# Kernel optimization log

Hardware: AMD Instinct MI355X
Metric: run time of the kernel (lower is better)

## Reference

```python
import jax, jax.numpy as jnp
import numpy as np

BATCH, LENGTH, IN, STATE, OUT = 8, 4096, 512, 256, 512


def setup_inputs() -> dict:
    key = jax.random.key(0)
    k1, k2, k3, k4, k5 = jax.random.split(key, 5)
    u = jax.random.normal(k1, (BATCH, LENGTH, IN), dtype=jnp.float32)
    x0 = jax.random.normal(k2, (BATCH, STATE), dtype=jnp.float32)
    A = 0.9999 * (2.0 * jax.random.uniform(k3, (STATE,), dtype=jnp.float32) - 1.0)
    B = jax.random.normal(k4, (IN, STATE), dtype=jnp.float32) / (STATE + IN) ** 0.5
    C = jax.random.normal(k5, (STATE, OUT), dtype=jnp.float32) / STATE ** 0.5
    return {"u": u, "x0": x0, "A": A, "B": B, "C": C}


def reference(u, x0, A, B, C):
    L = u.shape[1]
    # A_powers[t, n] = A[n] ** t, shape [L, state]
    A_powers = jnp.power(A[None, :], jnp.arange(L, dtype=u.dtype)[:, None])
    uB = u @ B  # [batch, L, state]
    # FFT convolution; inputs are real so rfft/irfft gives same result as
    # real(ifft(fft*fft)) in the original.
    T = 2 ** int(np.ceil(np.log2(2 * L - 1)))
    Af = jnp.fft.rfft(A_powers, n=T, axis=0)  # [T/2+1, state]
    Uf = jnp.fft.rfft(uB, n=T, axis=1)        # [batch, T/2+1, state]
    x = jnp.fft.irfft(Af[None, :, :] * Uf, n=T, axis=1)[:, :L]  # [batch, L, state]
    # initial-state contribution: A * A_powers * x0
    x = x + A[None, None, :] * A_powers[None, :, :] * x0[:, None, :]
    y = x @ C  # [batch, L, out]
    return (y, x[:, -1])
```

## Files before the change

### kernel.cpp

```cpp
#include <hip/hip_runtime.h>

#define BATCH   8
#define LENGTH  4096
#define IN_DIM  512
#define STATE   256
#define OUT_DIM 512
#define NC      256
#define LC      16

typedef __attribute__((ext_vector_type(8))) short bf16x8;
typedef __attribute__((ext_vector_type(4))) float f32x4;
typedef __attribute__((ext_vector_type(4))) unsigned short u16x4;

union FragU { bf16x8 v; unsigned u[4]; };

__device__ __forceinline__ unsigned short bf16_rne(float v) {
    unsigned u = __builtin_bit_cast(unsigned, v);
    unsigned r = (u + 0x7FFFu + ((u >> 16) & 1u)) >> 16;
    return (unsigned short)r;
}
__device__ __forceinline__ float bf16_f(unsigned short h) {
    unsigned u = ((unsigned)h) << 16;
    return __builtin_bit_cast(float, u);
}

__global__ __launch_bounds__(256) void split_weights(
    const float* __restrict__ B, const float* __restrict__ C,
    unsigned short* __restrict__ Bhi, unsigned short* __restrict__ Blo,
    unsigned short* __restrict__ Chi, unsigned short* __restrict__ Clo)
{
    int id = blockIdx.x * 256 + threadIdx.x;
    if (id < IN_DIM * STATE) {
        int k = id & (IN_DIM - 1), n = id >> 9;
        float v = B[(size_t)k * STATE + n];
        unsigned short h = bf16_rne(v);
        Bhi[id] = h;
        Blo[id] = bf16_rne(v - bf16_f(h));
    } else {
        int id2 = id - IN_DIM * STATE;
        int k = id2 & (STATE - 1), n = id2 >> 8;
        float v = C[(size_t)k * OUT_DIM + n];
        unsigned short h = bf16_rne(v);
        Chi[id2] = h;
        Clo[id2] = bf16_rne(v - bf16_f(h));
    }
}

__global__ __launch_bounds__(512, 4) void gemm_dbuf(
    const float* __restrict__ Af, const unsigned short* __restrict__ Bthi,
    const unsigned short* __restrict__ Btlo, float* __restrict__ Cc,
    int N_, int K)
{
    __shared__ unsigned short lds[2 * 16384];

    const int tid  = threadIdx.x;
    const int wave = tid >> 6;
    const int lane = tid & 63;
    const int n0 = blockIdx.x * 128;
    const int m0 = blockIdx.y * 128;

    const char* gp[4];
    int ldsoff[4], gstep[4];
    #pragma unroll
    for (int t = 0; t < 4; ++t) {
        int gi = wave * 4 + t;
        if (gi < 16) {
            int p = gi * 64 + lane;
            int row = p >> 3, s = p & 7;
            int l = s ^ (row & 7);
            gp[t] = (const char*)(Af + (size_t)(m0 + row) * K + l * 4);
            gstep[t] = 32 * 4;
            ldsoff[t] = gi * 512;
        } else {
            int q2 = (gi - 16) >> 3;
            int pi = gi & 7;
            int p = pi * 64 + lane;
            int row = p >> 2, s = p & 3;
            int l = s ^ ((row >> 1) & 3);
            const unsigned short* base = q2 ? Btlo : Bthi;
            gp[t] = (const char*)(base + (size_t)(n0 + row) * K + l * 8);
            gstep[t] = 32 * 2;
            ldsoff[t] = 8192 + q2 * 4096 + pi * 512;
        }
    }

    const int r = lane & 15, q = lane >> 4;
    const int wm = (wave >> 1) * 32, wn = (wave & 1) * 64;

    int aoff[2][2], boff[4];
    #pragma unroll
    for (int i = 0; i < 2; ++i) {
        int row = wm + i * 16 + r;
        #pragma unroll
        for (int h = 0; h < 2; ++h)
            aoff[i][h] = row * 64 + ((2 * q + h) ^ (row & 7)) * 8;
    }
    #pragma unroll
    for (int j = 0; j < 4; ++j) {
        int row = wn + j * 16 + r;
        boff[j] = row * 32 + (q ^ ((row >> 1) & 3)) * 8;
    }

    f32x4 acc[2][4];
    #pragma unroll
    for (int i = 0; i < 2; ++i)
        #pragma unroll
        for (int j = 0; j < 4; ++j)
            acc[i][j] = (f32x4){0.f, 0.f, 0.f, 0.f};

    #pragma unroll
    for (int t = 0; t < 4; ++t) {
        __builtin_amdgcn_global_load_lds(
            (const __attribute__((address_space(1))) unsigned*)(gp[t]),
            (__attribute__((address_space(3))) unsigned*)(&lds[ldsoff[t]]),
            16, 0, 0);
        gp[t] += gstep[t];
    }

    const int nit = K >> 5;
    for (int it = 0; it < nit; ++it) {
        asm volatile("" ::: "memory");
        __builtin_amdgcn_s_barrier();
        asm volatile("" ::: "memory");
        if (it + 1 < nit) {
            const int bb = ((it + 1) & 1) * 16384;
            #pragma unroll
            for (int t = 0; t < 4; ++t) {
                __builtin_amdgcn_global_load_lds(
                    (const __attribute__((address_space(1))) unsigned*)(gp[t]),
                    (__attribute__((address_space(3))) unsigned*)(&lds[bb + ldsoff[t]]),
                    16, 0, 0);
                gp[t] += gstep[t];
            }
            __builtin_amdgcn_s_waitcnt(0x0F74);
        } else {
            __builtin_amdgcn_s_waitcnt(0x0F70);
        }
        asm volatile("" ::: "memory");
        __builtin_amdgcn_s_barrier();
        asm volatile("" ::: "memory");

        const unsigned short* buf = &lds[(it & 1) * 16384];

        FragU ahi[2], alo[2];
        #pragma unroll
        for (int i = 0; i < 2; ++i) {
            #pragma unroll
            for (int h = 0; h < 2; ++h) {
                float4 f = *(const float4*)(buf + aoff[i][h]);
                unsigned bx = __builtin_bit_cast(unsigned, f.x);
                unsigned by = __builtin_bit_cast(unsigned, f.y);
                unsigned bz = __builtin_bit_cast(unsigned, f.z);
                unsigned bw = __builtin_bit_cast(unsigned, f.w);
                ahi[i].u[h * 2]     = __builtin_amdgcn_perm(by, bx, 0x07060302);
                ahi[i].u[h * 2 + 1] = __builtin_amdgcn_perm(bw, bz, 0x07060302);
                float lx = f.x - __builtin_bit_cast(float, bx & 0xFFFF0000u);
                float ly = f.y - __builtin_bit_cast(float, by & 0xFFFF0000u);
                float lz = f.z - __builtin_bit_cast(float, bz & 0xFFFF0000u);
                float lw = f.w - __builtin_bit_cast(float, bw & 0xFFFF0000u);
                alo[i].u[h * 2]     = __builtin_amdgcn_perm(
                    __builtin_bit_cast(unsigned, ly), __builtin_bit_cast(unsigned, lx), 0x07060302);
                alo[i].u[h * 2 + 1] = __builtin_amdgcn_perm(
                    __builtin_bit_cast(unsigned, lw), __builtin_bit_cast(unsigned, lz), 0x07060302);
            }
        }
        FragU bhi[4], blo[4];
        #pragma unroll
        for (int j = 0; j < 4; ++j) {
            bhi[j].v = *(const bf16x8*)(buf +  8192 + boff[j]);
            blo[j].v = *(const bf16x8*)(buf + 12288 + boff[j]);
        }
        #pragma unroll
        for (int i = 0; i < 2; ++i)
            #pragma unroll
            for (int j = 0; j < 4; ++j) {
                acc[i][j] = __builtin_amdgcn_mfma_f32_16x16x32_bf16(ahi[i].v, bhi[j].v, acc[i][j], 0, 0, 0);
                acc[i][j] = __builtin_amdgcn_mfma_f32_16x16x32_bf16(alo[i].v, bhi[j].v, acc[i][j], 0, 0, 0);
                acc[i][j] = __builtin_amdgcn_mfma_f32_16x16x32_bf16(ahi[i].v, blo[j].v, acc[i][j], 0, 0, 0);
            }
    }

    #pragma unroll
    for (int i = 0; i < 2; ++i) {
        #pragma unroll
        for (int reg = 0; reg < 4; ++reg) {
            int mg = m0 + wm + i * 16 + q * 4 + reg;
            float* dst = Cc + (size_t)mg * N_ + n0 + wn + r;
            dst[0]  = acc[i][0][reg];
            dst[16] = acc[i][1][reg];
            dst[32] = acc[i][2][reg];
            dst[48] = acc[i][3][reg];
        }
    }
}

__global__ __launch_bounds__(512, 4) void gemm_presplit(
    const unsigned short* __restrict__ Athi, const unsigned short* __restrict__ Atlo,
    const unsigned short* __restrict__ Bthi, const unsigned short* __restrict__ Btlo,
    float* __restrict__ Cc, int N_, int K)
{
    __shared__ unsigned short lds[2 * 16384];

    const int tid  = threadIdx.x;
    const int wave = tid >> 6;
    const int lane = tid & 63;
    const int n0 = blockIdx.x * 128;
    const int m0 = blockIdx.y * 128;

    const char* gp[4];
    int ldsoff[4];
    #pragma unroll
    for (int t = 0; t < 4; ++t) {
        int gi = wave * 4 + t;
        int plane = gi >> 3;
        int pi = gi & 7;
        int p = pi * 64 + lane;
        int row = p >> 2, s = p & 3;
        int l = s ^ ((row >> 1) & 3);
        const unsigned short* base =
            (plane == 0) ? Athi : (plane == 1) ? Atlo : (plane == 2) ? Bthi : Btlo;
        int r0 = (plane < 2) ? m0 : n0;
        gp[t] = (const char*)(base + (size_t)(r0 + row) * K + l * 8);
        ldsoff[t] = plane * 4096 + pi * 512;
    }

    const int r = lane & 15, q = lane >> 4;
    const int wm = (wave >> 2) * 64, wn = (wave & 3) * 32;

    int aoff[4], boff[2];
    #pragma unroll
    for (int i = 0; i < 4; ++i) {
        int row = wm + i * 16 + r;
        aoff[i] = row * 32 + (q ^ ((row >> 1) & 3)) * 8;
    }
    #pragma unroll
    for (int j = 0; j < 2; ++j) {
        int row = wn + j * 16 + r;
        boff[j] = row * 32 + (q ^ ((row >> 1) & 3)) * 8;
    }

    f32x4 acc[4][2];
    #pragma unroll
    for (int i = 0; i < 4; ++i)
        #pragma unroll
        for (int j = 0; j < 2; ++j)
            acc[i][j] = (f32x4){0.f, 0.f, 0.f, 0.f};

    #pragma unroll
    for (int t = 0; t < 4; ++t) {
        __builtin_amdgcn_global_load_lds(
            (const __attribute__((address_space(1))) unsigned*)(gp[t]),
            (__attribute__((address_space(3))) unsigned*)(&lds[ldsoff[t]]),
            16, 0, 0);
        gp[t] += 64;
    }

    const int nit = K >> 5;
    for (int it = 0; it < nit; ++it) {
        asm volatile("" ::: "memory");
        __builtin_amdgcn_s_barrier();
        asm volatile("" ::: "memory");
        if (it + 1 < nit) {
            const int bb = ((it + 1) & 1) * 16384;
            #pragma unroll
            for (int t = 0; t < 4; ++t) {
                __builtin_amdgcn_global_load_lds(
                    (const __attribute__((address_space(1))) unsigned*)(gp[t]),
                    (__attribute__((address_space(3))) unsigned*)(&lds[bb + ldsoff[t]]),
                    16, 0, 0);
                gp[t] += 64;
            }
            __builtin_amdgcn_s_waitcnt(0x0F74);
        } else {
            __builtin_amdgcn_s_waitcnt(0x0F70);
        }
        asm volatile("" ::: "memory");
        __builtin_amdgcn_s_barrier();
        asm volatile("" ::: "memory");

        const unsigned short* buf = &lds[(it & 1) * 16384];

        FragU ahi[4], alo[4];
        #pragma unroll
        for (int i = 0; i < 4; ++i) {
            ahi[i].v = *(const bf16x8*)(buf +        aoff[i]);
            alo[i].v = *(const bf16x8*)(buf + 4096 + aoff[i]);
        }
        FragU bhi[2], blo[2];
        #pragma unroll
        for (int j = 0; j < 2; ++j) {
            bhi[j].v = *(const bf16x8*)(buf +  8192 + boff[j]);
            blo[j].v = *(const bf16x8*)(buf + 12288 + boff[j]);
        }
        #pragma unroll
        for (int i = 0; i < 4; ++i)
            #pragma unroll
            for (int j = 0; j < 2; ++j) {
                acc[i][j] = __builtin_amdgcn_mfma_f32_16x16x32_bf16(ahi[i].v, bhi[j].v, acc[i][j], 0, 0, 0);
                acc[i][j] = __builtin_amdgcn_mfma_f32_16x16x32_bf16(alo[i].v, bhi[j].v, acc[i][j], 0, 0, 0);
                acc[i][j] = __builtin_amdgcn_mfma_f32_16x16x32_bf16(ahi[i].v, blo[j].v, acc[i][j], 0, 0, 0);
            }
    }

    #pragma unroll
    for (int i = 0; i < 4; ++i) {
        #pragma unroll
        for (int reg = 0; reg < 4; ++reg) {
            int mg = m0 + wm + i * 16 + q * 4 + reg;
            float* dst = Cc + (size_t)mg * N_ + n0 + wn + r;
            dst[0]  = acc[i][0][reg];
            dst[16] = acc[i][1][reg];
        }
    }
}

__global__ __launch_bounds__(64) void scan_carry(
    const float* __restrict__ uB, const float* __restrict__ A,
    float* __restrict__ carry)
{
    const int b = blockIdx.x;
    const int c = blockIdx.y;
    const int t = threadIdx.x;
    const float4 a = *(const float4*)(A + 4 * t);
    const float4* p = (const float4*)(uB + ((size_t)b * LENGTH + (size_t)c * LC) * STATE) + t;
    float4 s = make_float4(0.f, 0.f, 0.f, 0.f);
    #pragma unroll
    for (int j = 0; j < LC; ++j) {
        float4 v = p[(size_t)j * (STATE / 4)];
        s.x = fmaf(a.x, s.x, v.x);
        s.y = fmaf(a.y, s.y, v.y);
        s.z = fmaf(a.z, s.z, v.z);
        s.w = fmaf(a.w, s.w, v.w);
    }
    *((float4*)(carry + ((size_t)b * NC + c) * STATE) + t) = s;
}

__global__ __launch_bounds__(256) void scan_entries(
    const float* __restrict__ carry, const float* __restrict__ A,
    const float* __restrict__ x0, float* __restrict__ entry)
{
    const int b = blockIdx.x;
    const int n = threadIdx.x;
    const float a = A[n];
    float aL = a;
    #pragma unroll
    for (int k = 0; k < 4; ++k) aL *= aL;

    float s = x0[(size_t)b * STATE + n];
    const float* cr = carry + (size_t)b * NC * STATE + n;
    float* en = entry + (size_t)b * NC * STATE + n;
    #pragma unroll 8
    for (int c = 0; c < NC; ++c) {
        en[(size_t)c * STATE] = s;
        s = fmaf(aL, s, cr[(size_t)c * STATE]);
    }
}

__global__ __launch_bounds__(64) void scan_apply(
    const float* __restrict__ uB, const float* __restrict__ A,
    const float* __restrict__ entry,
    unsigned short* __restrict__ xhi, unsigned short* __restrict__ xlo,
    float* __restrict__ x_last)
{
    const int b = blockIdx.x;
    const int c = blockIdx.y;
    const int t = threadIdx.x;
    const float4 a = *(const float4*)(A + 4 * t);

    float4 s = *((const float4*)(entry + ((size_t)b * NC + c) * STATE) + t);

    const size_t base = ((size_t)b * LENGTH + (size_t)c * LC) * STATE;
    const float4* p = (const float4*)(uB + base) + t;
    u16x4* qh = (u16x4*)(xhi + base) + t;
    u16x4* ql = (u16x4*)(xlo + base) + t;
    #pragma unroll
    for (int j = 0; j < LC; ++j) {
        float4 v = p[(size_t)j * (STATE / 4)];
        s.x = fmaf(a.x, s.x, v.x);
        s.y = fmaf(a.y, s.y, v.y);
        s.z = fmaf(a.z, s.z, v.z);
        s.w = fmaf(a.w, s.w, v.w);
        u16x4 hh, ll;
        unsigned ux = __builtin_bit_cast(unsigned, s.x);
        unsigned uy = __builtin_bit_cast(unsigned, s.y);
        unsigned uz = __builtin_bit_cast(unsigned, s.z);
        unsigned uw = __builtin_bit_cast(unsigned, s.w);
        hh[0] = (unsigned short)(ux >> 16);
        hh[1] = (unsigned short)(uy >> 16);
        hh[2] = (unsigned short)(uz >> 16);
        hh[3] = (unsigned short)(uw >> 16);
        float lx = s.x - __builtin_bit_cast(float, ux & 0xFFFF0000u);
        float ly = s.y - __builtin_bit_cast(float, uy & 0xFFFF0000u);
        float lz = s.z - __builtin_bit_cast(float, uz & 0xFFFF0000u);
        float lw = s.w - __builtin_bit_cast(float, uw & 0xFFFF0000u);
        ll[0] = (unsigned short)(__builtin_bit_cast(unsigned, lx) >> 16);
        ll[1] = (unsigned short)(__builtin_bit_cast(unsigned, ly) >> 16);
        ll[2] = (unsigned short)(__builtin_bit_cast(unsigned, lz) >> 16);
        ll[3] = (unsigned short)(__builtin_bit_cast(unsigned, lw) >> 16);
        qh[(size_t)j * (STATE / 4)] = hh;
        ql[(size_t)j * (STATE / 4)] = ll;
    }
    if (c == NC - 1)
        *((float4*)(x_last + (size_t)b * STATE) + t) = s;
}

extern "C" void kernel_launch(void* const* d_in, const int* in_sizes, int n_in,
                              void* d_out, int out_size, void* d_ws, size_t ws_size,
                              hipStream_t stream)
{
    const float* u  = (const float*)d_in[0];
    const float* x0 = (const float*)d_in[1];
    const float* A  = (const float*)d_in[2];
    const float* B  = (const float*)d_in[3];
    const float* C  = (const float*)d_in[4];

    const size_t MB = 1024 * 1024;
    char* ws = (char*)d_ws;

    unsigned short* xhi = (unsigned short*)(ws);
    unsigned short* xlo = (unsigned short*)(ws + 16 * MB);
    float* carry = (float*)(ws + 32 * MB);
    float* entry = (float*)(ws + 34 * MB);
    unsigned short* Bt_hi = (unsigned short*)(ws + 36 * MB);
    unsigned short* Bt_lo = (unsigned short*)(ws + 36 * MB + 256 * 1024);
    unsigned short* Ct_hi = (unsigned short*)(ws + 36 * MB + 512 * 1024);
    unsigned short* Ct_lo = (unsigned short*)(ws + 36 * MB + 768 * 1024);

    float* y      = (float*)d_out;
    float* x_last = y + (size_t)BATCH * LENGTH * OUT_DIM;
    float* uB     = (float*)((char*)d_out + 32 * MB);

    const int M = BATCH * LENGTH;

    split_weights<<<dim3((IN_DIM * STATE + STATE * OUT_DIM) / 256), dim3(256), 0, stream>>>(
        B, C, Bt_hi, Bt_lo, Ct_hi, Ct_lo);

    gemm_dbuf<<<dim3(STATE / 128, M / 128), dim3(512), 0, stream>>>(
        u, Bt_hi, Bt_lo, uB, STATE, IN_DIM);

    scan_carry<<<dim3(BATCH, NC), dim3(64), 0, stream>>>(uB, A, carry);
    scan_entries<<<dim3(BATCH), dim3(256), 0, stream>>>(carry, A, x0, entry);
    scan_apply<<<dim3(BATCH, NC), dim3(64), 0, stream>>>(uB, A, entry, xhi, xlo, x_last);

    gemm_presplit<<<dim3(OUT_DIM / 128, M / 128), dim3(512), 0, stream>>>(
        xhi, xlo, Ct_hi, Ct_lo, y, OUT_DIM, STATE);
}
```

Baseline: 208.7 us.

## Fuse chunk-carry scan reduction into uB GEMM epilogue; prefetch uB in scan_apply

Computes the per-chunk scan carries directly from the GEMM accumulators in the gemm_dbuf epilogue. Each 16-row chunk is weighted by powers of A and reduced across lanes with shuffles, which removes the separate scan_carry kernel and its full re-read of uB. scan_apply now loads all 16 uB rows into registers before the recurrence so the loads can be in flight together. The cost is extra epilogue work and register pressure in the GEMM, more registers in scan_apply, and summation-order differences in the carries.

```diff
diff --git a/kernel.cpp b/kernel.cpp
--- a/kernel.cpp
+++ b/kernel.cpp
@@ -49,6 +49,7 @@
 __global__ __launch_bounds__(512, 4) void gemm_dbuf(
     const float* __restrict__ Af, const unsigned short* __restrict__ Bthi,
     const unsigned short* __restrict__ Btlo, float* __restrict__ Cc,
+    const float* __restrict__ Av, float* __restrict__ carry,
     int N_, int K)
 {
     __shared__ unsigned short lds[2 * 16384];
@@ -192,6 +193,28 @@
             dst[48] = acc[i][3][reg];
         }
     }
+
+    {
+        const int b  = m0 >> 12;
+        const int c0 = ((m0 & 4095) + wm) >> 4;
+        #pragma unroll
+        for (int j = 0; j < 4; ++j) {
+            const int n = n0 + wn + j * 16 + r;
+            const float a  = Av[n];
+            const float a2 = a * a, a3 = a2 * a, a4 = a2 * a2;
+            const float a8 = a4 * a4, a12 = a8 * a4;
+            const float base = (q == 0) ? a12 : (q == 1) ? a8 : (q == 2) ? a4 : 1.f;
+            #pragma unroll
+            for (int i = 0; i < 2; ++i) {
+                float partial = base * (a3 * acc[i][j][0] + a2 * acc[i][j][1]
+                                      + a  * acc[i][j][2] +      acc[i][j][3]);
+                partial += __shfl_xor(partial, 16);
+                partial += __shfl_xor(partial, 32);
+                if (q == 0)
+                    carry[((size_t)b * NC + (c0 + i)) * STATE + n] = partial;
+            }
+        }
+    }
 }
 
 __global__ __launch_bounds__(512, 4) void gemm_presplit(
@@ -314,27 +337,6 @@
     }
 }
 
-__global__ __launch_bounds__(64) void scan_carry(
-    const float* __restrict__ uB, const float* __restrict__ A,
-    float* __restrict__ carry)
-{
-    const int b = blockIdx.x;
-    const int c = blockIdx.y;
-    const int t = threadIdx.x;
-    const float4 a = *(const float4*)(A + 4 * t);
-    const float4* p = (const float4*)(uB + ((size_t)b * LENGTH + (size_t)c * LC) * STATE) + t;
-    float4 s = make_float4(0.f, 0.f, 0.f, 0.f);
-    #pragma unroll
-    for (int j = 0; j < LC; ++j) {
-        float4 v = p[(size_t)j * (STATE / 4)];
-        s.x = fmaf(a.x, s.x, v.x);
-        s.y = fmaf(a.y, s.y, v.y);
-        s.z = fmaf(a.z, s.z, v.z);
-        s.w = fmaf(a.w, s.w, v.w);
-    }
-    *((float4*)(carry + ((size_t)b * NC + c) * STATE) + t) = s;
-}
-
 __global__ __launch_bounds__(256) void scan_entries(
     const float* __restrict__ carry, const float* __restrict__ A,
     const float* __restrict__ x0, float* __restrict__ entry)
@@ -367,19 +369,23 @@
     const int t = threadIdx.x;
     const float4 a = *(const float4*)(A + 4 * t);
 
-    float4 s = *((const float4*)(entry + ((size_t)b * NC + c) * STATE) + t);
-
     const size_t base = ((size_t)b * LENGTH + (size_t)c * LC) * STATE;
     const float4* p = (const float4*)(uB + base) + t;
+
+    float4 v[LC];
+    #pragma unroll
+    for (int j = 0; j < LC; ++j) v[j] = p[(size_t)j * (STATE / 4)];
+
+    float4 s = *((const float4*)(entry + ((size_t)b * NC + c) * STATE) + t);
+
     u16x4* qh = (u16x4*)(xhi + base) + t;
     u16x4* ql = (u16x4*)(xlo + base) + t;
     #pragma unroll
     for (int j = 0; j < LC; ++j) {
-        float4 v = p[(size_t)j * (STATE / 4)];
-        s.x = fmaf(a.x, s.x, v.x);
-        s.y = fmaf(a.y, s.y, v.y);
-        s.z = fmaf(a.z, s.z, v.z);
-        s.w = fmaf(a.w, s.w, v.w);
+        s.x = fmaf(a.x, s.x, v[j].x);
+        s.y = fmaf(a.y, s.y, v[j].y);
+        s.z = fmaf(a.z, s.z, v[j].z);
+        s.w = fmaf(a.w, s.w, v[j].w);
         u16x4 hh, ll;
         unsigned ux = __builtin_bit_cast(unsigned, s.x);
         unsigned uy = __builtin_bit_cast(unsigned, s.y);
@@ -436,9 +442,8 @@
         B, C, Bt_hi, Bt_lo, Ct_hi, Ct_lo);
 
     gemm_dbuf<<<dim3(STATE / 128, M / 128), dim3(512), 0, stream>>>(
-        u, Bt_hi, Bt_lo, uB, STATE, IN_DIM);
-
-    scan_carry<<<dim3(BATCH, NC), dim3(64), 0, stream>>>(uB, A, carry);
+        u, Bt_hi, Bt_lo, uB, A, carry, STATE, IN_DIM);
+
     scan_entries<<<dim3(BATCH), dim3(256), 0, stream>>>(carry, A, x0, entry);
     scan_apply<<<dim3(BATCH, NC), dim3(64), 0, stream>>>(uB, A, entry, xhi, xlo, x_last);
 
```

Result: no change. 205.8 us (-1.4%).
